# Optimization experiments

Hardware: AMD Instinct MI355X
Metric: run time of the kernel (lower is better)

Reference implementation:

```python
import jax, jax.numpy as jnp
import numpy as np

D_MODEL = 256
N_HEADS = 8
N_LEVELS = 4
N_POINTS = 4
SHAPES = [(128, 128), (64, 64), (32, 32), (16, 16)]  # (H, W) per level


def _query_hw(Lq):
    h = int(Lq ** 0.5)
    w = Lq // h
    if h * w != Lq:
        facs = [(i, Lq // i) for i in range(1, int(Lq ** 0.5) + 1) if Lq % i == 0]
        h, w = min(facs, key=lambda t: abs(t[0] - t[1]))
    return h, w


def _grid_sample(img, grid):
    # img: [B, D, H, W]; grid: [B, Lq, P, 2] in [-1,1] (x, y)
    # bilinear, padding_mode='zeros', align_corners=False
    B, D, H, W = img.shape
    gx, gy = grid[..., 0], grid[..., 1]
    x = ((gx + 1.0) * W - 1.0) * 0.5
    y = ((gy + 1.0) * H - 1.0) * 0.5
    x0 = jnp.floor(x)
    y0 = jnp.floor(y)
    wx1 = x - x0
    wy1 = y - y0
    wx0 = 1.0 - wx1
    wy0 = 1.0 - wy1
    x0i = x0.astype(jnp.int32)
    y0i = y0.astype(jnp.int32)
    x1i = x0i + 1
    y1i = y0i + 1
    img_flat = img.reshape(B, D, H * W)

    def gather(yi, xi):
        valid = (xi >= 0) & (xi < W) & (yi >= 0) & (yi < H)
        idx = jnp.clip(yi, 0, H - 1) * W + jnp.clip(xi, 0, W - 1)  # [B,Lq,P]
        v = jnp.take_along_axis(img_flat, idx.reshape(B, 1, -1), axis=2)
        v = v.reshape(B, D, *yi.shape[1:])  # [B,D,Lq,P]
        return v * valid[:, None].astype(img.dtype)

    return (gather(y0i, x0i) * (wy0 * wx0)[:, None]
            + gather(y0i, x1i) * (wy0 * wx1)[:, None]
            + gather(y1i, x0i) * (wy1 * wx0)[:, None]
            + gather(y1i, x1i) * (wy1 * wx1)[:, None])


def _forward(query, input_flatten, spatial_shapes,
             W_off, b_off, W_attn, b_attn, W_val, b_val, W_out, b_out):
    N, Lq, C = query.shape
    M, L, P = N_HEADS, N_LEVELS, N_POINTS
    D = C // M
    shapes = np.asarray(spatial_shapes)  # static

    value = (input_flatten @ W_val + b_val).reshape(N, -1, M, D)
    off = (query @ W_off + b_off).reshape(N, Lq, M, L, P, 2)
    attn = jax.nn.softmax((query @ W_attn + b_attn).reshape(N, Lq, M, L * P), axis=-1)
    attn = attn.reshape(N, Lq, M, L, P)

    # normalized reference grid derived from Len_q (2D branch)
    qh, qw = _query_hw(Lq)
    ry, rx = jnp.meshgrid(jnp.linspace(0.5, qh - 0.5, qh) / qh,
                          jnp.linspace(0.5, qw - 0.5, qw) / qw, indexing='ij')
    ref = jnp.stack([rx.reshape(-1), ry.reshape(-1)], axis=-1)  # [Lq, 2] (x,y)
    norm = jnp.asarray(np.stack([shapes[:, 1], shapes[:, 0]], -1), jnp.float32)  # [L,2]=(W,H)
    loc = ref[None, :, None, None, None, :] + off / norm[None, None, None, :, None, :]
    grids = 2.0 * loc - 1.0  # [N,Lq,M,L,P,2]

    starts = np.concatenate([[0], np.cumsum(shapes[:, 0] * shapes[:, 1])])
    sampled = []
    for l in range(L):
        H, W = int(shapes[l, 0]), int(shapes[l, 1])
        v = value[:, starts[l]:starts[l + 1]]            # [N, H*W, M, D]
        v = v.transpose(0, 2, 3, 1).reshape(N * M, D, H, W)
        g = grids[:, :, :, l].transpose(0, 2, 1, 3, 4).reshape(N * M, Lq, P, 2)
        sampled.append(_grid_sample(v, g))               # [NM, D, Lq, P]

    vals = jnp.stack(sampled, axis=-2)                   # [NM, D, Lq, L, P]
    # faithful to original: values flattened (P, L)-major, weights (L, P)-major
    vals = vals.transpose(0, 1, 2, 4, 3).reshape(N * M, D, Lq, P * L)
    w = attn.transpose(0, 2, 1, 3, 4).reshape(N * M, 1, Lq, L * P)
    out = (vals * w).sum(-1).reshape(N, M * D, Lq).transpose(0, 2, 1)  # [N,Lq,C]
    return out @ W_out + b_out


def setup_inputs():
    key = jax.random.key(0)
    ks = jax.random.split(key, 12)
    N, Lq, C = 2, 16384, D_MODEL
    M, L, P = N_HEADS, N_LEVELS, N_POINTS
    Lin = sum(h * w for h, w in SHAPES)
    s = 0.02
    # sampling_offsets bias: original directional grid init
    thetas = np.arange(M, dtype=np.float32) * (2.0 * np.pi / M)
    gi = np.stack([np.cos(thetas), np.sin(thetas)], -1)
    gi = gi / np.abs(gi).max(-1, keepdims=True)
    gi = np.tile(gi.reshape(M, 1, 1, 2), (1, L, P, 1))
    for i in range(P):
        gi[:, :, i, :] *= (i + 1)
    inp = {
        'query': jax.random.normal(ks[0], (N, Lq, C), jnp.float32),
        'reference_points': jax.random.uniform(ks[1], (N, Lq, L, 2), jnp.float32),
        'input_flatten': jax.random.normal(ks[2], (N, Lin, C), jnp.float32),
        'spatial_shapes': jnp.array(SHAPES, jnp.int32),
        'level_start_index': jnp.array(np.concatenate([[0], np.cumsum([h * w for h, w in SHAPES[:-1]])]), jnp.int32),
        'W_off': jax.random.normal(ks[3], (C, M * L * P * 2), jnp.float32) * s,
        'b_off': jnp.asarray(gi.reshape(-1), jnp.float32),
        'W_attn': jax.random.normal(ks[4], (C, M * L * P), jnp.float32) * s,
        'b_attn': jnp.zeros((M * L * P,), jnp.float32),
        'W_val': jax.random.normal(ks[5], (C, C), jnp.float32) * (1.0 / np.sqrt(C)),
        'b_val': jnp.zeros((C,), jnp.float32),
        'W_out': jax.random.normal(ks[6], (C, C), jnp.float32) * (1.0 / np.sqrt(C)),
        'b_out': jnp.zeros((C,), jnp.float32),
    }
    return inp


def reference(query, reference_points, input_flatten, spatial_shapes, level_start_index,
              W_off, b_off, W_attn, b_attn, W_val, b_val, W_out, b_out):
    assert reference_points.shape[-1] == 2
    return _forward(query, input_flatten, spatial_shapes,
                    W_off, b_off, W_attn, b_attn, W_val, b_val, W_out, b_out)
```

## Files before the change

### kernel.cpp

```cpp
#include <hip/hip_runtime.h>
#include <math.h>

#define NB   2
#define LQ   16384
#define CDIM 256
#define MH   8
#define DH   32
#define LIN  21760
#define NPIX (NB * LIN)

typedef __attribute__((ext_vector_type(8))) _Float16 f16x8;
typedef __attribute__((ext_vector_type(4))) _Float16 f16x4;
typedef __attribute__((ext_vector_type(4))) float    f32x4;

__device__ __forceinline__ void async16(const void* g, void* l) {
    __builtin_amdgcn_global_load_lds(
        (const __attribute__((address_space(1))) void*)g,
        (__attribute__((address_space(3))) void*)l,
        16, 0, 0);
}

__global__ __launch_bounds__(256) void tsplit_all_kernel(
    const float* __restrict__ Wv, const float* __restrict__ Wo,
    const float* __restrict__ Wf, const float* __restrict__ Wa,
    _Float16* __restrict__ Wvt, _Float16* __restrict__ Wot, _Float16* __restrict__ Wct)
{
    const int i = blockIdx.x * 256 + threadIdx.x;
    const int r = i >> 8;
    const int kk = i & 255;
    if (r < 256) {
        Wvt[r * 256 + kk] = (_Float16)Wv[kk * 256 + r];
    } else if (r < 512) {
        const int n = r - 256;
        Wot[n * 256 + kk] = (_Float16)Wo[kk * 256 + n];
    } else if (r < 768) {
        const int n = r - 512;
        Wct[n * 256 + kk] = (_Float16)Wf[kk * 256 + n];
    } else {
        const int n = r - 768;
        Wct[(256 + n) * 256 + kk] = (_Float16)Wa[kk * 128 + n];
    }
}

template <int OUT_MODE, bool A_F32>
__global__ __launch_bounds__(256) void gemm_f16(
    const void* __restrict__ Araw, const _Float16* __restrict__ Bt,
    const float* __restrict__ bias0, const float* __restrict__ bias1,
    void* __restrict__ C0, void* __restrict__ C1,
    int M, int N, int K, int N0)
{
    __shared__ __align__(16) char AshRaw[2][A_F32 ? 128 * 32 * 4 : 128 * 32 * 2];
    __shared__ __align__(16) _Float16 Bsh[2][128 * 32];

    const int tid  = threadIdx.x;
    const int wave = tid >> 6, lane = tid & 63;
    const int quad = lane >> 4, l16 = lane & 15;
    const int bm = blockIdx.y * 128;
    const int bn = blockIdx.x * 128;
    const int wrow = wave * 32;

    f32x4 acc[2][8] = {};

    const int sB0 = tid, sB1 = tid + 256;
    const int rB0 = sB0 >> 2, rB1 = sB1 >> 2;
    const int kB0 = ((sB0 & 3) ^ ((rB0 >> 1) & 3)) << 3;
    const int kB1 = ((sB1 & 3) ^ ((rB1 >> 1) & 3)) << 3;

    const int T = K >> 5;
    int cur = 0;

    auto stage = [&](int buf, int k0) {
        if (A_F32) {
            const float* A = (const float*)Araw;
            float* AshF = (float*)AshRaw[buf];
            #pragma unroll
            for (int j = 0; j < 4; ++j) {
                const int s = tid + 256 * j;
                const int row = s >> 3;
                const int kg = ((s & 7) ^ (row & 7)) << 2;
                async16(A + (size_t)(bm + row) * K + k0 + kg, AshF + s * 4);
            }
        } else {
            const _Float16* A = (const _Float16*)Araw;
            _Float16* Ash = (_Float16*)AshRaw[buf];
            async16(A + (size_t)(bm + rB0) * K + k0 + kB0, Ash + sB0 * 8);
            async16(A + (size_t)(bm + rB1) * K + k0 + kB1, Ash + sB1 * 8);
        }
        async16(Bt + (size_t)(bn + rB0) * K + k0 + kB0, Bsh[buf] + sB0 * 8);
        async16(Bt + (size_t)(bn + rB1) * K + k0 + kB1, Bsh[buf] + sB1 * 8);
    };

    stage(0, 0);
    __syncthreads();

    for (int t = 0; t < T; ++t) {
        if (t + 1 < T) stage(cur ^ 1, (t + 1) << 5);

        f16x8 ah[2];
        #pragma unroll
        for (int r = 0; r < 2; ++r) {
            const int arow = wrow + r * 16 + l16;
            if (A_F32) {
                const float* AshF = (const float*)AshRaw[cur];
                const int c0 = (2 * quad)     ^ (arow & 7);
                const int c1 = (2 * quad + 1) ^ (arow & 7);
                const f32x4 a0 = *(const f32x4*)&AshF[arow * 32 + c0 * 4];
                const f32x4 a1 = *(const f32x4*)&AshF[arow * 32 + c1 * 4];
                f16x8 h;
                h[0] = (_Float16)a0[0]; h[1] = (_Float16)a0[1];
                h[2] = (_Float16)a0[2]; h[3] = (_Float16)a0[3];
                h[4] = (_Float16)a1[0]; h[5] = (_Float16)a1[1];
                h[6] = (_Float16)a1[2]; h[7] = (_Float16)a1[3];
                ah[r] = h;
            } else {
                const _Float16* Ash = (const _Float16*)AshRaw[cur];
                ah[r] = *(const f16x8*)&Ash[arow * 32 + ((quad ^ ((arow >> 1) & 3)) << 3)];
            }
        }
        #pragma unroll
        for (int half = 0; half < 2; ++half) {
            f16x8 bh[4];
            #pragma unroll
            for (int c = 0; c < 4; ++c) {
                const int brow = half * 64 + c * 16 + l16;
                bh[c] = *(const f16x8*)&Bsh[cur][brow * 32 + ((quad ^ ((brow >> 1) & 3)) << 3)];
            }
            #pragma unroll
            for (int r = 0; r < 2; ++r)
                #pragma unroll
                for (int c = 0; c < 4; ++c)
                    acc[r][half * 4 + c] = __builtin_amdgcn_mfma_f32_16x16x32_f16(
                        bh[c], ah[r], acc[r][half * 4 + c], 0, 0, 0);
        }
        __syncthreads();
        cur ^= 1;
    }

    void* Cb; const float* bb; int ldc, coff;
    if (bn < N0) { Cb = C0; bb = bias0; ldc = N0;     coff = 0;  }
    else         { Cb = C1; bb = bias1; ldc = N - N0; coff = N0; }
    #pragma unroll
    for (int cidx = 0; cidx < 8; ++cidx) {
        const int col = bn + cidx * 16 + quad * 4 - coff;
        const float4 bia = *(const float4*)&bb[col];
        #pragma unroll
        for (int r = 0; r < 2; ++r) {
            const int rr = bm + wrow + r * 16 + l16;
            float4 v;
            v.x = acc[r][cidx][0] + bia.x;
            v.y = acc[r][cidx][1] + bia.y;
            v.z = acc[r][cidx][2] + bia.z;
            v.w = acc[r][cidx][3] + bia.w;
            if (OUT_MODE == 0) {
                *(float4*)&((float*)Cb)[(size_t)rr * ldc + col] = v;
            } else if (OUT_MODE == 1) {
                f16x4 h;
                h[0] = (_Float16)v.x; h[1] = (_Float16)v.y;
                h[2] = (_Float16)v.z; h[3] = (_Float16)v.w;
                *(f16x4*)&((_Float16*)Cb)[(size_t)rr * ldc + col] = h;
            } else {
                f16x4 h;
                h[0] = (_Float16)v.x; h[1] = (_Float16)v.y;
                h[2] = (_Float16)v.z; h[3] = (_Float16)v.w;
                *(f16x4*)&((_Float16*)Cb)[((size_t)(col >> 5) * NPIX + rr) * 32 + (col & 31)] = h;
            }
        }
    }
}

__global__ __launch_bounds__(256) void sample_kernel_v9(
    const _Float16* __restrict__ value,
    const float* __restrict__ off,
    const float* __restrict__ attn,
    _Float16* __restrict__ outv)
{
    __shared__ __align__(16) float lds_task[8][516];

    const int tid = threadIdx.x;
    const int qbase = blockIdx.x * 4;

    #pragma unroll
    for (int j = 0; j < 2; ++j) {
        const int t  = tid + 256 * j;
        const int q  = t >> 7;
        const int m  = (t >> 4) & 7;
        const int pt = t & 15;
        const int l  = pt >> 2;
        const int p  = pt & 3;
        const int qi = qbase + q;
        const int lq = qi & (LQ - 1);
        const int n  = qi >> 14;

        const int Hl = 128 >> l;
        const int STARTS[4] = {0, 16384, 20480, 21504};

        const float2 oxy = *(const float2*)&off[(size_t)qi * 256 + m * 32 + pt * 2];

        const float logit = attn[(size_t)qi * 128 + m * 16 + p * 4 + l];
        float mx = logit;
        #pragma unroll
        for (int d = 1; d < 16; d <<= 1) mx = fmaxf(mx, __shfl_xor(mx, d, 16));
        const float e = __expf(logit - mx);
        float sm = e;
        #pragma unroll
        for (int d = 1; d < 16; d <<= 1) sm += __shfl_xor(sm, d, 16);
        const float w = e / sm;

        const float refx = ((lq & 127) + 0.5f) * (1.0f / 128.0f);
        const float refy = ((lq >> 7)  + 0.5f) * (1.0f / 128.0f);

        const float x = refx * (float)Hl + oxy.x - 0.5f;
        const float y = refy * (float)Hl + oxy.y - 0.5f;
        const float x0f = floorf(x), y0f = floorf(y);
        const int x0 = (int)x0f, y0 = (int)y0f;
        const int x1 = x0 + 1,  y1 = y0 + 1;
        const float fx = x - x0f, fy = y - y0f;
        const float gx = 1.f - fx, gy = 1.f - fy;

        const float vx0 = (x0 >= 0 && x0 < Hl) ? 1.f : 0.f;
        const float vx1 = (x1 >= 0 && x1 < Hl) ? 1.f : 0.f;
        const float vy0 = (y0 >= 0 && y0 < Hl) ? 1.f : 0.f;
        const float vy1 = (y1 >= 0 && y1 < Hl) ? 1.f : 0.f;

        const int x0c = min(max(x0, 0), Hl - 1);
        const int x1c = min(max(x1, 0), Hl - 1);
        const int y0c = min(max(y0, 0), Hl - 1);
        const int y1c = min(max(y1, 0), Hl - 1);

        const int baseb = m * (NPIX * 64) + (n * LIN + STARTS[l]) * 64;
        const int i00 = baseb + (y0c * Hl + x0c) * 64;
        const int i01 = baseb + (y0c * Hl + x1c) * 64;
        const int i10 = baseb + (y1c * Hl + x0c) * 64;
        const int i11 = baseb + (y1c * Hl + x1c) * 64;

        float4 wv;
        wv.x = w * gy * gx * vy0 * vx0;
        wv.y = w * gy * fx * vy0 * vx1;
        wv.z = w * fy * gx * vy1 * vx0;
        wv.w = w * fy * fx * vy1 * vx1;

        float* dst = &lds_task[m][(q * 16 + pt) * 8];
        int4 iv = {i00, i01, i10, i11};
        *(int4*)dst = iv;
        *(float4*)(dst + 4) = wv;
    }
    __syncthreads();

    const int q  = tid >> 6;
    const int m  = (tid >> 3) & 7;
    const int d4 = tid & 7;
    const int qi = qbase + q;
    const unsigned dd = (unsigned)(d4 * 8);
    const char* vp = (const char*)value;

    f32x4 acc = {0.f, 0.f, 0.f, 0.f};
    #pragma unroll
    for (int pt = 0; pt < 16; ++pt) {
        const float* td = &lds_task[m][(q * 16 + pt) * 8];
        const int4  iv = *(const int4*)td;
        const float4 wv = *(const float4*)(td + 4);
        const f16x4 v00 = *(const f16x4*)(vp + ((unsigned)iv.x + dd));
        const f16x4 v01 = *(const f16x4*)(vp + ((unsigned)iv.y + dd));
        const f16x4 v10 = *(const f16x4*)(vp + ((unsigned)iv.z + dd));
        const f16x4 v11 = *(const f16x4*)(vp + ((unsigned)iv.w + dd));
        f32x4 f00 = {(float)v00[0], (float)v00[1], (float)v00[2], (float)v00[3]};
        f32x4 f01 = {(float)v01[0], (float)v01[1], (float)v01[2], (float)v01[3]};
        f32x4 f10 = {(float)v10[0], (float)v10[1], (float)v10[2], (float)v10[3]};
        f32x4 f11 = {(float)v11[0], (float)v11[1], (float)v11[2], (float)v11[3]};
        acc += wv.x * f00 + wv.y * f01 + wv.z * f10 + wv.w * f11;
    }

    f16x4 o;
    o[0] = (_Float16)acc[0]; o[1] = (_Float16)acc[1];
    o[2] = (_Float16)acc[2]; o[3] = (_Float16)acc[3];
    *(f16x4*)&outv[(size_t)qi * 256 + m * 32 + d4 * 4] = o;
}

extern "C" void kernel_launch(void* const* d_in, const int* in_sizes, int n_in,
                              void* d_out, int out_size, void* d_ws, size_t ws_size,
                              hipStream_t stream)
{
    const float* query         = (const float*)d_in[0];
    const float* input_flatten = (const float*)d_in[2];
    const float* W_off  = (const float*)d_in[5];
    const float* b_off  = (const float*)d_in[6];
    const float* W_attn = (const float*)d_in[7];
    const float* b_attn = (const float*)d_in[8];
    const float* W_val  = (const float*)d_in[9];
    const float* b_val  = (const float*)d_in[10];
    const float* W_out  = (const float*)d_in[11];
    const float* b_out  = (const float*)d_in[12];
    float* out = (float*)d_out;

    char* w = (char*)d_ws;
    _Float16* Sf16 = (_Float16*)w;
    _Float16* value16 = (_Float16*)(w + 23068672);
    float*    attnbuf = (float*)(w + 67633152);
    _Float16* Wvt = (_Float16*)(w + 84410368);
    _Float16* Wot = Wvt + 65536;
    _Float16* Wct = Wot + 65536;
    float* offbuf = out;

    dim3 blk(256);

    tsplit_all_kernel<<<896, blk, 0, stream>>>(W_val, W_out, W_off, W_attn, Wvt, Wot, Wct);

    gemm_f16<2, true><<<dim3(2, 340), blk, 0, stream>>>(
        input_flatten, Wvt, b_val, b_val, value16, value16, 43520, 256, 256, 256);

    gemm_f16<0, true><<<dim3(3, 256), blk, 0, stream>>>(
        query, Wct, b_off, b_attn, offbuf, attnbuf, 32768, 384, 256, 256);

    sample_kernel_v9<<<8192, blk, 0, stream>>>(value16, offbuf, attnbuf, Sf16);

    gemm_f16<0, false><<<dim3(2, 256), blk, 0, stream>>>(
        Sf16, Wot, b_out, b_out, out, out, 32768, 256, 256, 256);
}
```

Baseline: 258.4 us.

## Merge projection GEMMs, stage full K in LDS, widen sampler loads

The two input projection GEMMs are merged into one launch that picks its problem by block index. All GEMMs now stage the full K=256 slice of B (and of A, in f32 halves) into LDS with an XOR swizzle, replacing the double-buffered K=32 pipeline and cutting the number of barriers. The sampling kernel handles 8 queries per block, loads 8 halfs per lane per corner instead of 4, and stores its LDS task table in swizzled int4/float4 arrays. The large LDS footprint (about 128 KB per block) lowers occupancy, and with no prefetch overlap, loads are no longer hidden behind compute.

```diff
diff --git a/kernel.cpp b/kernel.cpp
--- a/kernel.cpp
+++ b/kernel.cpp
@@ -42,100 +42,12 @@
     }
 }
 
-template <int OUT_MODE, bool A_F32>
-__global__ __launch_bounds__(256) void gemm_f16(
-    const void* __restrict__ Araw, const _Float16* __restrict__ Bt,
-    const float* __restrict__ bias0, const float* __restrict__ bias1,
-    void* __restrict__ C0, void* __restrict__ C1,
-    int M, int N, int K, int N0)
-{
-    __shared__ __align__(16) char AshRaw[2][A_F32 ? 128 * 32 * 4 : 128 * 32 * 2];
-    __shared__ __align__(16) _Float16 Bsh[2][128 * 32];
-
-    const int tid  = threadIdx.x;
-    const int wave = tid >> 6, lane = tid & 63;
-    const int quad = lane >> 4, l16 = lane & 15;
-    const int bm = blockIdx.y * 128;
-    const int bn = blockIdx.x * 128;
-    const int wrow = wave * 32;
-
-    f32x4 acc[2][8] = {};
-
-    const int sB0 = tid, sB1 = tid + 256;
-    const int rB0 = sB0 >> 2, rB1 = sB1 >> 2;
-    const int kB0 = ((sB0 & 3) ^ ((rB0 >> 1) & 3)) << 3;
-    const int kB1 = ((sB1 & 3) ^ ((rB1 >> 1) & 3)) << 3;
-
-    const int T = K >> 5;
-    int cur = 0;
-
-    auto stage = [&](int buf, int k0) {
-        if (A_F32) {
-            const float* A = (const float*)Araw;
-            float* AshF = (float*)AshRaw[buf];
-            #pragma unroll
-            for (int j = 0; j < 4; ++j) {
-                const int s = tid + 256 * j;
-                const int row = s >> 3;
-                const int kg = ((s & 7) ^ (row & 7)) << 2;
-                async16(A + (size_t)(bm + row) * K + k0 + kg, AshF + s * 4);
-            }
-        } else {
-            const _Float16* A = (const _Float16*)Araw;
-            _Float16* Ash = (_Float16*)AshRaw[buf];
-            async16(A + (size_t)(bm + rB0) * K + k0 + kB0, Ash + sB0 * 8);
-            async16(A + (size_t)(bm + rB1) * K + k0 + kB1, Ash + sB1 * 8);
-        }
-        async16(Bt + (size_t)(bn + rB0) * K + k0 + kB0, Bsh[buf] + sB0 * 8);
-        async16(Bt + (size_t)(bn + rB1) * K + k0 + kB1, Bsh[buf] + sB1 * 8);
-    };
-
-    stage(0, 0);
-    __syncthreads();
-
-    for (int t = 0; t < T; ++t) {
-        if (t + 1 < T) stage(cur ^ 1, (t + 1) << 5);
-
-        f16x8 ah[2];
-        #pragma unroll
-        for (int r = 0; r < 2; ++r) {
-            const int arow = wrow + r * 16 + l16;
-            if (A_F32) {
-                const float* AshF = (const float*)AshRaw[cur];
-                const int c0 = (2 * quad)     ^ (arow & 7);
-                const int c1 = (2 * quad + 1) ^ (arow & 7);
-                const f32x4 a0 = *(const f32x4*)&AshF[arow * 32 + c0 * 4];
-                const f32x4 a1 = *(const f32x4*)&AshF[arow * 32 + c1 * 4];
-                f16x8 h;
-                h[0] = (_Float16)a0[0]; h[1] = (_Float16)a0[1];
-                h[2] = (_Float16)a0[2]; h[3] = (_Float16)a0[3];
-                h[4] = (_Float16)a1[0]; h[5] = (_Float16)a1[1];
-                h[6] = (_Float16)a1[2]; h[7] = (_Float16)a1[3];
-                ah[r] = h;
-            } else {
-                const _Float16* Ash = (const _Float16*)AshRaw[cur];
-                ah[r] = *(const f16x8*)&Ash[arow * 32 + ((quad ^ ((arow >> 1) & 3)) << 3)];
-            }
-        }
-        #pragma unroll
-        for (int half = 0; half < 2; ++half) {
-            f16x8 bh[4];
-            #pragma unroll
-            for (int c = 0; c < 4; ++c) {
-                const int brow = half * 64 + c * 16 + l16;
-                bh[c] = *(const f16x8*)&Bsh[cur][brow * 32 + ((quad ^ ((brow >> 1) & 3)) << 3)];
-            }
-            #pragma unroll
-            for (int r = 0; r < 2; ++r)
-                #pragma unroll
-                for (int c = 0; c < 4; ++c)
-                    acc[r][half * 4 + c] = __builtin_amdgcn_mfma_f32_16x16x32_f16(
-                        bh[c], ah[r], acc[r][half * 4 + c], 0, 0, 0);
-        }
-        __syncthreads();
-        cur ^= 1;
-    }
-
+
+template <int OUT_MODE>
+__device__ __forceinline__ void gemm_epilogue(
+    f32x4 (&acc)[2][8], int bm, int bn, int wave, int quad, int l16,
+    const float* bias0, const float* bias1, void* C0, void* C1, int N, int N0)
+{
     void* Cb; const float* bb; int ldc, coff;
     if (bn < N0) { Cb = C0; bb = bias0; ldc = N0;     coff = 0;  }
     else         { Cb = C1; bb = bias1; ldc = N - N0; coff = N0; }
@@ -145,7 +57,7 @@
         const float4 bia = *(const float4*)&bb[col];
         #pragma unroll
         for (int r = 0; r < 2; ++r) {
-            const int rr = bm + wrow + r * 16 + l16;
+            const int rr = bm + wave * 32 + r * 16 + l16;
             float4 v;
             v.x = acc[r][cidx][0] + bia.x;
             v.y = acc[r][cidx][1] + bia.y;
@@ -153,11 +65,6 @@
             v.w = acc[r][cidx][3] + bia.w;
             if (OUT_MODE == 0) {
                 *(float4*)&((float*)Cb)[(size_t)rr * ldc + col] = v;
-            } else if (OUT_MODE == 1) {
-                f16x4 h;
-                h[0] = (_Float16)v.x; h[1] = (_Float16)v.y;
-                h[2] = (_Float16)v.z; h[3] = (_Float16)v.w;
-                *(f16x4*)&((_Float16*)Cb)[(size_t)rr * ldc + col] = h;
             } else {
                 f16x4 h;
                 h[0] = (_Float16)v.x; h[1] = (_Float16)v.y;
@@ -168,19 +75,170 @@
     }
 }
 
-__global__ __launch_bounds__(256) void sample_kernel_v9(
+__device__ __forceinline__ void stage_B(const _Float16* __restrict__ Bt, int bn,
+                                        _Float16* Bsh, int tid)
+{
+    #pragma unroll
+    for (int j = 0; j < 16; ++j) {
+        const int s = tid + 256 * j;
+        const int row = s >> 5, phys = s & 31;
+        const int cl = phys ^ (row & 7);
+        async16(Bt + (size_t)(bn + row) * 256 + cl * 8, Bsh + s * 8);
+    }
+}
+
+__device__ __forceinline__ void mfma_step(const _Float16* Bsh, const f16x8 (&ah)[2],
+                                          int t, int quad, int l16, f32x4 (&acc)[2][8])
+{
+    #pragma unroll
+    for (int half = 0; half < 2; ++half) {
+        f16x8 bh[4];
+        #pragma unroll
+        for (int c = 0; c < 4; ++c) {
+            const int brow = half * 64 + c * 16 + l16;
+            const int pb = (t * 4 + quad) ^ (brow & 7);
+            bh[c] = *(const f16x8*)&Bsh[brow * 256 + pb * 8];
+        }
+        #pragma unroll
+        for (int r = 0; r < 2; ++r)
+            #pragma unroll
+            for (int c = 0; c < 4; ++c)
+                acc[r][half * 4 + c] = __builtin_amdgcn_mfma_f32_16x16x32_f16(
+                    bh[c], ah[r], acc[r][half * 4 + c], 0, 0, 0);
+    }
+}
+
+__device__ __forceinline__ void core_f16(
+    const _Float16* __restrict__ A, const _Float16* __restrict__ Bt,
+    int bm, int bn, _Float16* Ash, _Float16* Bsh, f32x4 (&acc)[2][8])
+{
+    const int tid = threadIdx.x;
+    const int wave = tid >> 6, lane = tid & 63;
+    const int quad = lane >> 4, l16 = lane & 15;
+    stage_B(Bt, bn, Bsh, tid);
+    #pragma unroll
+    for (int j = 0; j < 16; ++j) {
+        const int s = tid + 256 * j;
+        const int row = s >> 5, phys = s & 31;
+        const int cl = phys ^ (row & 7);
+        async16(A + (size_t)(bm + row) * 256 + cl * 8, Ash + s * 8);
+    }
+    __syncthreads();
+    #pragma unroll
+    for (int t = 0; t < 8; ++t) {
+        f16x8 ah[2];
+        #pragma unroll
+        for (int r = 0; r < 2; ++r) {
+            const int arow = wave * 32 + r * 16 + l16;
+            const int pa = (t * 4 + quad) ^ (arow & 7);
+            ah[r] = *(const f16x8*)&Ash[arow * 256 + pa * 8];
+        }
+        mfma_step(Bsh, ah, t, quad, l16, acc);
+    }
+}
+
+__device__ __forceinline__ void core_f32(
+    const float* __restrict__ A, const _Float16* __restrict__ Bt,
+    int bm, int bn, float* AshF, _Float16* Bsh, f32x4 (&acc)[2][8])
+{
+    const int tid = threadIdx.x;
+    const int wave = tid >> 6, lane = tid & 63;
+    const int quad = lane >> 4, l16 = lane & 15;
+    stage_B(Bt, bn, Bsh, tid);
+    #pragma unroll
+    for (int h = 0; h < 2; ++h) {
+        #pragma unroll
+        for (int j = 0; j < 16; ++j) {
+            const int s = tid + 256 * j;
+            const int row = s >> 5, phys = s & 31;
+            const int cl = phys ^ (row & 7);
+            async16(A + (size_t)(bm + row) * 256 + h * 128 + cl * 4, AshF + s * 4);
+        }
+        __syncthreads();
+        #pragma unroll
+        for (int tt = 0; tt < 4; ++tt) {
+            const int t = h * 4 + tt;
+            f16x8 ah[2];
+            #pragma unroll
+            for (int r = 0; r < 2; ++r) {
+                const int arow = wave * 32 + r * 16 + l16;
+                const int cl0 = tt * 8 + quad * 2;
+                const int p0 = cl0       ^ (arow & 7);
+                const int p1 = (cl0 + 1) ^ (arow & 7);
+                const f32x4 a0 = *(const f32x4*)&AshF[arow * 128 + p0 * 4];
+                const f32x4 a1 = *(const f32x4*)&AshF[arow * 128 + p1 * 4];
+                f16x8 hh;
+                hh[0] = (_Float16)a0[0]; hh[1] = (_Float16)a0[1];
+                hh[2] = (_Float16)a0[2]; hh[3] = (_Float16)a0[3];
+                hh[4] = (_Float16)a1[0]; hh[5] = (_Float16)a1[1];
+                hh[6] = (_Float16)a1[2]; hh[7] = (_Float16)a1[3];
+                ah[r] = hh;
+            }
+            mfma_step(Bsh, ah, t, quad, l16, acc);
+        }
+        if (h == 0) __syncthreads();
+    }
+}
+
+__global__ __launch_bounds__(256) void gemm12_fullk(
+    const float* __restrict__ IF, const float* __restrict__ Q,
+    const _Float16* __restrict__ Wvt, const _Float16* __restrict__ Wct,
+    const float* __restrict__ b_val, const float* __restrict__ b_off,
+    const float* __restrict__ b_attn,
+    _Float16* __restrict__ value16, float* __restrict__ offbuf, float* __restrict__ attnbuf)
+{
+    __shared__ __align__(16) float    AshF[128 * 128];
+    __shared__ __align__(16) _Float16 Bsh[128 * 256];
+    f32x4 acc[2][8] = {};
+    const int tid = threadIdx.x;
+    const int wave = tid >> 6, lane = tid & 63;
+    const int quad = lane >> 4, l16 = lane & 15;
+    const int bid = blockIdx.x;
+
+    if (bid < 680) {
+        const int bm = (bid >> 1) * 128, bn = (bid & 1) * 128;
+        core_f32(IF, Wvt, bm, bn, AshF, Bsh, acc);
+        gemm_epilogue<2>(acc, bm, bn, wave, quad, l16,
+                         b_val, b_val, value16, value16, 256, 256);
+    } else {
+        const int r = bid - 680;
+        const int bm = (r / 3) * 128, bn = (r % 3) * 128;
+        core_f32(Q, Wct, bm, bn, AshF, Bsh, acc);
+        gemm_epilogue<0>(acc, bm, bn, wave, quad, l16,
+                         b_off, b_attn, offbuf, attnbuf, 384, 256);
+    }
+}
+
+__global__ __launch_bounds__(256) void gemm3_fullk(
+    const _Float16* __restrict__ A, const _Float16* __restrict__ Wot,
+    const float* __restrict__ b_out, float* __restrict__ out)
+{
+    __shared__ __align__(16) _Float16 Ash[128 * 256];
+    __shared__ __align__(16) _Float16 Bsh[128 * 256];
+    f32x4 acc[2][8] = {};
+    const int tid = threadIdx.x;
+    const int wave = tid >> 6, lane = tid & 63;
+    const int quad = lane >> 4, l16 = lane & 15;
+    const int bm = blockIdx.y * 128, bn = blockIdx.x * 128;
+    core_f16(A, Wot, bm, bn, Ash, Bsh, acc);
+    gemm_epilogue<0>(acc, bm, bn, wave, quad, l16,
+                     b_out, b_out, out, out, 256, 256);
+}
+
+__global__ __launch_bounds__(256) void sample_kernel_v10(
     const _Float16* __restrict__ value,
     const float* __restrict__ off,
     const float* __restrict__ attn,
     _Float16* __restrict__ outv)
 {
-    __shared__ __align__(16) float lds_task[8][516];
-
-    const int tid = threadIdx.x;
-    const int qbase = blockIdx.x * 4;
-
-    #pragma unroll
-    for (int j = 0; j < 2; ++j) {
+    __shared__ __align__(16) int4   ivt[128][8];
+    __shared__ __align__(16) float4 wvt[128][8];
+
+    const int tid = threadIdx.x;
+    const int qbase = blockIdx.x * 8;
+
+    #pragma unroll
+    for (int j = 0; j < 4; ++j) {
         const int t  = tid + 256 * j;
         const int q  = t >> 7;
         const int m  = (t >> 4) & 7;
@@ -239,41 +297,49 @@
         wv.z = w * fy * gx * vy1 * vx0;
         wv.w = w * fy * fx * vy1 * vx1;
 
-        float* dst = &lds_task[m][(q * 16 + pt) * 8];
+        const int cc = m ^ (pt & 7);
         int4 iv = {i00, i01, i10, i11};
-        *(int4*)dst = iv;
-        *(float4*)(dst + 4) = wv;
+        ivt[q * 16 + pt][cc] = iv;
+        wvt[q * 16 + pt][cc] = wv;
     }
     __syncthreads();
 
-    const int q  = tid >> 6;
-    const int m  = (tid >> 3) & 7;
-    const int d4 = tid & 7;
+    const int q  = tid >> 5;
+    const int m  = (tid >> 2) & 7;
+    const int d8 = tid & 3;
     const int qi = qbase + q;
-    const unsigned dd = (unsigned)(d4 * 8);
+    const unsigned dd = (unsigned)(d8 * 16);
     const char* vp = (const char*)value;
 
-    f32x4 acc = {0.f, 0.f, 0.f, 0.f};
+    f32x4 accL = {0.f, 0.f, 0.f, 0.f};
+    f32x4 accH = {0.f, 0.f, 0.f, 0.f};
     #pragma unroll
     for (int pt = 0; pt < 16; ++pt) {
-        const float* td = &lds_task[m][(q * 16 + pt) * 8];
-        const int4  iv = *(const int4*)td;
-        const float4 wv = *(const float4*)(td + 4);
-        const f16x4 v00 = *(const f16x4*)(vp + ((unsigned)iv.x + dd));
-        const f16x4 v01 = *(const f16x4*)(vp + ((unsigned)iv.y + dd));
-        const f16x4 v10 = *(const f16x4*)(vp + ((unsigned)iv.z + dd));
-        const f16x4 v11 = *(const f16x4*)(vp + ((unsigned)iv.w + dd));
-        f32x4 f00 = {(float)v00[0], (float)v00[1], (float)v00[2], (float)v00[3]};
-        f32x4 f01 = {(float)v01[0], (float)v01[1], (float)v01[2], (float)v01[3]};
-        f32x4 f10 = {(float)v10[0], (float)v10[1], (float)v10[2], (float)v10[3]};
-        f32x4 f11 = {(float)v11[0], (float)v11[1], (float)v11[2], (float)v11[3]};
-        acc += wv.x * f00 + wv.y * f01 + wv.z * f10 + wv.w * f11;
-    }
-
-    f16x4 o;
-    o[0] = (_Float16)acc[0]; o[1] = (_Float16)acc[1];
-    o[2] = (_Float16)acc[2]; o[3] = (_Float16)acc[3];
-    *(f16x4*)&outv[(size_t)qi * 256 + m * 32 + d4 * 4] = o;
+        const int cc = m ^ (pt & 7);
+        const int4  iv = ivt[q * 16 + pt][cc];
+        const float4 wv = wvt[q * 16 + pt][cc];
+        const f16x8 v00 = *(const f16x8*)(vp + ((unsigned)iv.x + dd));
+        const f16x8 v01 = *(const f16x8*)(vp + ((unsigned)iv.y + dd));
+        const f16x8 v10 = *(const f16x8*)(vp + ((unsigned)iv.z + dd));
+        const f16x8 v11 = *(const f16x8*)(vp + ((unsigned)iv.w + dd));
+        f32x4 l00 = {(float)v00[0], (float)v00[1], (float)v00[2], (float)v00[3]};
+        f32x4 h00 = {(float)v00[4], (float)v00[5], (float)v00[6], (float)v00[7]};
+        f32x4 l01 = {(float)v01[0], (float)v01[1], (float)v01[2], (float)v01[3]};
+        f32x4 h01 = {(float)v01[4], (float)v01[5], (float)v01[6], (float)v01[7]};
+        f32x4 l10 = {(float)v10[0], (float)v10[1], (float)v10[2], (float)v10[3]};
+        f32x4 h10 = {(float)v10[4], (float)v10[5], (float)v10[6], (float)v10[7]};
+        f32x4 l11 = {(float)v11[0], (float)v11[1], (float)v11[2], (float)v11[3]};
+        f32x4 h11 = {(float)v11[4], (float)v11[5], (float)v11[6], (float)v11[7]};
+        accL += wv.x * l00 + wv.y * l01 + wv.z * l10 + wv.w * l11;
+        accH += wv.x * h00 + wv.y * h01 + wv.z * h10 + wv.w * h11;
+    }
+
+    f16x8 o;
+    o[0] = (_Float16)accL[0]; o[1] = (_Float16)accL[1];
+    o[2] = (_Float16)accL[2]; o[3] = (_Float16)accL[3];
+    o[4] = (_Float16)accH[0]; o[5] = (_Float16)accH[1];
+    o[6] = (_Float16)accH[2]; o[7] = (_Float16)accH[3];
+    *(f16x8*)&outv[(size_t)qi * 256 + m * 32 + d8 * 8] = o;
 }
 
 extern "C" void kernel_launch(void* const* d_in, const int* in_sizes, int n_in,
@@ -305,14 +371,11 @@
 
     tsplit_all_kernel<<<896, blk, 0, stream>>>(W_val, W_out, W_off, W_attn, Wvt, Wot, Wct);
 
-    gemm_f16<2, true><<<dim3(2, 340), blk, 0, stream>>>(
-        input_flatten, Wvt, b_val, b_val, value16, value16, 43520, 256, 256, 256);
-
-    gemm_f16<0, true><<<dim3(3, 256), blk, 0, stream>>>(
-        query, Wct, b_off, b_attn, offbuf, attnbuf, 32768, 384, 256, 256);
-
-    sample_kernel_v9<<<8192, blk, 0, stream>>>(value16, offbuf, attnbuf, Sf16);
-
-    gemm_f16<0, false><<<dim3(2, 256), blk, 0, stream>>>(
-        Sf16, Wot, b_out, b_out, out, out, 32768, 256, 256, 256);
-}
+    gemm12_fullk<<<1448, blk, 0, stream>>>(
+        input_flatten, query, Wvt, Wct, b_val, b_off, b_attn,
+        value16, offbuf, attnbuf);
+
+    sample_kernel_v10<<<4096, blk, 0, stream>>>(value16, offbuf, attnbuf, Sf16);
+
+    gemm3_fullk<<<dim3(2, 256), blk, 0, stream>>>(Sf16, Wot, b_out, out);
+}
```

New measurement: 237.3 us. -8.2%, faster.
